# Kernel tuning notes

Measured on AMD Instinct MI355X. Metric: run time of the kernel, lower is better.

The kernel has to match this reference:

```python
import jax, jax.numpy as jnp
import numpy as np

B, D_IN, H, D_OUT = 1024, 64, 128, 16


def setup_inputs() -> dict:
    key = jax.random.key(0)
    k0, k1, k2 = jax.random.split(key, 3)
    x = jax.random.normal(k0, (B, D_IN), dtype=jnp.float32)
    W1 = jax.random.normal(k1, (D_IN, H), dtype=jnp.float32) / np.sqrt(D_IN).astype(np.float32)
    b1 = jnp.zeros((H,), dtype=jnp.float32)
    W2 = jax.random.normal(k2, (H, D_OUT), dtype=jnp.float32) / np.sqrt(H).astype(np.float32)
    b2 = jnp.zeros((D_OUT,), dtype=jnp.float32)
    return {"x": x, "W1": W1, "b1": b1, "W2": W2, "b2": b2}


def reference(x, W1, b1, W2, b2):
    # Wrapped net: 2-layer tanh MLP (hessQuik NN equivalent).
    def f_single(xi):  # xi: [D_IN] -> [D_OUT]
        return jnp.tanh(xi @ W1 + b1) @ W2 + b2

    # f: [B, D_OUT]  (torch: f.view(B, -1))
    f = jax.vmap(f_single)(x)

    # Torch builds df[b, i, j] = d f_j / d x_i via one grad per output column;
    # one reverse sweep per output == jacrev, vmapped over batch.
    J = jax.vmap(jax.jacrev(f_single))(x)            # [B, D_OUT, D_IN]
    df = jnp.transpose(J, (0, 2, 1))                 # [B, D_IN, D_OUT]

    # Torch builds d2f[b, k, i, j] = d^2 f_j / (d x_k d x_i); symmetric in (k, i).
    Hs = jax.vmap(jax.hessian(f_single))(x)          # [B, D_OUT, D_IN, D_IN]
    d2f = jnp.transpose(Hs, (0, 2, 3, 1))            # [B, D_IN, D_IN, D_OUT]

    return f, df, d2f
```

## Files before the change

kernel.cpp:

```cpp
#include <hip/hip_runtime.h>
#include <hip/hip_bf16.h>


typedef unsigned short u16;
typedef short s8v __attribute__((ext_vector_type(8)));
typedef float f4v __attribute__((ext_vector_type(4)));

__device__ __forceinline__ u16 f2bf(float f){
  __hip_bfloat16 h = __float2bfloat16(f);
  return __builtin_bit_cast(u16, h);
}

#define W1S 132

__global__ __launch_bounds__(256) void k_all(
    const float* __restrict__ x, const float* __restrict__ W1, const float* __restrict__ b1,
    const float* __restrict__ W2, const float* __restrict__ b2,
    float* __restrict__ f_out, float* __restrict__ df_out, float* __restrict__ d2f)
{
  const int tid  = threadIdx.x;
  const int lane = tid & 63;
  const int wave = tid >> 6;
  const int n = lane & 15;
  const int q = lane >> 4;
  const int b0 = blockIdx.x * 4;
  const int mb = blockIdx.y;

  __shared__ float sW1[64 * W1S];
  __shared__ __align__(16) float sGF[4096];
  __shared__ float sx[256];
  u16* sG = (u16*)sGF;

#pragma unroll
  for (int v = 0; v < 8; ++v){
    int idx = v*256 + tid;
    int r = idx >> 5;
    int c = (idx & 31) << 2;
    *(f4v*)&sW1[r*W1S + c] = *(const f4v*)&W1[r*128 + c];
  }
  sx[tid] = x[b0*64 + tid];
  __syncthreads();

  float a_keep = 0.f, s_keep = 0.f;
#pragma unroll
  for (int it = 0; it < 2; ++it){
    int idx = it*256 + tid;
    int s = idx >> 7;
    int h = idx & 127;
    float z = b1[h];
#pragma unroll 8
    for (int i = 0; i < 64; ++i) z += sx[s*64 + i] * sW1[i*W1S + h];
    float a = tanhf(z);
    float sd = 1.0f - a*a;
    float t = -2.0f * a * sd;
    if (it == mb){ a_keep = a; s_keep = sd; }
    f4v w2r[4];
#pragma unroll
    for (int v2 = 0; v2 < 4; ++v2) w2r[v2] = *(const f4v*)&W2[h*16 + v2*4];
#pragma unroll
    for (int j = 0; j < 16; ++j){
      int byte = (j*256 + h*2) ^ ((j & 7) << 4);
      sG[s*2048 + (byte >> 1)] = f2bf(t * w2r[j >> 2][j & 3]);
    }
  }
  __syncthreads();

  s8v bfrag[4][4];
#pragma unroll
  for (int s = 0; s < 4; ++s){
#pragma unroll
    for (int ks = 0; ks < 4; ++ks){
      int byte = (n*256 + q*16 + ks*64) ^ ((n & 7) << 4);
      bfrag[s][ks] = *(const s8v*)&sG[s*2048 + (byte >> 1)];
    }
  }
  __syncthreads();

  {
    const int ls = tid >> 7;
    const int h  = tid & 127;
    float* sF = sGF;
    sx[tid] = a_keep;
    f4v w2r[4];
#pragma unroll
    for (int v2 = 0; v2 < 4; ++v2) w2r[v2] = *(const f4v*)&W2[h*16 + v2*4];
#pragma unroll
    for (int v2 = 0; v2 < 4; ++v2){
      f4v sv;
#pragma unroll
      for (int e = 0; e < 4; ++e) sv[e] = s_keep * w2r[v2][e];
      *(f4v*)&sF[ls*2048 + h*16 + v2*4] = sv;
    }
    __syncthreads();

    const int sub = tid & 127;
    const int i   = sub >> 1;
    const int j0  = (sub & 1) * 8;
    const int bS  = b0 + 2*mb + ls;
    float acc[8] = {0,0,0,0,0,0,0,0};
    for (int h0 = 0; h0 < 128; h0 += 8){
      const float4* wp = (const float4*)&W1[i*128 + h0];
      float4 wa = wp[0], wb = wp[1];
      float wf[8] = {wa.x, wa.y, wa.z, wa.w, wb.x, wb.y, wb.z, wb.w};
#pragma unroll
      for (int hh = 0; hh < 8; ++hh){
        const f4v* sp = (const f4v*)&sF[ls*2048 + (h0 + hh)*16 + j0];
        f4v A = sp[0], Bv = sp[1];
        float w1 = wf[hh];
        acc[0] += w1*A[0];  acc[1] += w1*A[1];  acc[2] += w1*A[2];  acc[3] += w1*A[3];
        acc[4] += w1*Bv[0]; acc[5] += w1*Bv[1]; acc[6] += w1*Bv[2]; acc[7] += w1*Bv[3];
      }
    }
    f4v v0 = {acc[0], acc[1], acc[2], acc[3]};
    f4v v1 = {acc[4], acc[5], acc[6], acc[7]};
    float* dp = &df_out[bS*1024 + i*16 + j0];
    __builtin_nontemporal_store(v0, (f4v*)dp);
    __builtin_nontemporal_store(v1, (f4v*)(dp + 4));

    if (sub < 16){
      float accf = b2[sub];
      for (int h2 = 0; h2 < 128; ++h2) accf += sx[ls*128 + h2] * W2[h2*16 + sub];
      __builtin_nontemporal_store(accf, &f_out[bS*16 + sub]);
    }
  }

  const int R0 = mb*2048 + wave*512;
#pragma unroll 2
  for (int mt = 0; mt < 32; ++mt){
    const int rowbase = R0 + mt*16;
    const int r = rowbase + n;
    const int i = r & 63;
    const int k = r >> 6;
    const float* wi = &sW1[i*W1S];
    const float* wk = &sW1[k*W1S];
    s8v afrag[4];
#pragma unroll
    for (int ks = 0; ks < 4; ++ks){
      int c = q*8 + ks*32;
      f4v ia = *(const f4v*)&wi[c];
      f4v ib = *(const f4v*)&wi[c+4];
      f4v ka = *(const f4v*)&wk[c];
      f4v kb = *(const f4v*)&wk[c+4];
      s8v av;
#pragma unroll
      for (int e = 0; e < 4; ++e) av[e]   = (short)f2bf(ia[e]*ka[e]);
#pragma unroll
      for (int e = 0; e < 4; ++e) av[4+e] = (short)f2bf(ib[e]*kb[e]);
      afrag[ks] = av;
    }
#pragma unroll
    for (int s = 0; s < 4; ++s){
      f4v acc = {0.f, 0.f, 0.f, 0.f};
#pragma unroll
      for (int ks = 0; ks < 4; ++ks)
        acc = __builtin_amdgcn_mfma_f32_16x16x32_bf16(bfrag[s][ks], afrag[ks], acc, 0, 0, 0);
      float* op = d2f + (size_t)(b0 + s)*65536 + (size_t)(rowbase + n)*16 + q*4;
      *(f4v*)op = acc;
    }
  }
}

extern "C" void kernel_launch(void* const* d_in, const int* in_sizes, int n_in,
                              void* d_out, int out_size, void* d_ws, size_t ws_size,
                              hipStream_t stream)
{
  (void)in_sizes; (void)n_in; (void)out_size; (void)d_ws; (void)ws_size;
  const float* x  = (const float*)d_in[0];
  const float* W1 = (const float*)d_in[1];
  const float* b1 = (const float*)d_in[2];
  const float* W2 = (const float*)d_in[3];
  const float* b2 = (const float*)d_in[4];

  float* out     = (float*)d_out;
  float* f_out   = out;
  float* df_out  = out + 16384;
  float* d2f_out = out + 1064960;

  k_all<<<dim3(256, 2), 256, 0, stream>>>(x, W1, b1, W2, b2, f_out, df_out, d2f_out);
}
```

Baseline: 276.3 us.

## Exploit Hessian symmetry to compute only lower-triangular blocks and mirror stores

The d2f loop now computes only the diagonal and lower-triangular 16x16 (k,i) blocks, chosen from packed block tables. Off-diagonal results are written to both (k,i) and (i,k), which cuts MFMA and A-fragment work nearly in half. Each iteration also handles two adjacent k rows, sharing the i-row loads, and launch bounds now request two blocks per CU. The kernel appears bound by stores of the large d2f output, and the store volume is unchanged, so the compute savings may matter little. The mirrored stores are also less coalesced.

```diff
diff --git a/kernel.cpp b/kernel.cpp
--- a/kernel.cpp
+++ b/kernel.cpp
@@ -13,7 +13,7 @@
 
 #define W1S 132
 
-__global__ __launch_bounds__(256) void k_all(
+__global__ __launch_bounds__(256, 2) void k_all(
     const float* __restrict__ x, const float* __restrict__ W1, const float* __restrict__ b1,
     const float* __restrict__ W2, const float* __restrict__ b2,
     float* __restrict__ f_out, float* __restrict__ df_out, float* __restrict__ d2f)
@@ -124,38 +124,59 @@
     }
   }
 
-  const int R0 = mb*2048 + wave*512;
+  const int w8 = mb*4 + wave;
+  const size_t sB0 = (size_t)b0 * 65536;
 #pragma unroll 2
-  for (int mt = 0; mt < 32; ++mt){
-    const int rowbase = R0 + mt*16;
-    const int r = rowbase + n;
-    const int i = r & 63;
-    const int k = r >> 6;
-    const float* wi = &sW1[i*W1S];
-    const float* wk = &sW1[k*W1S];
-    s8v afrag[4];
+  for (int pp = 0; pp < 10; ++pp){
+    const int p   = w8*10 + pp;
+    const int blk = p >> 3;
+    const int kk2 = (p & 7) * 2;
+    const int KB  = (int)((0x2110003210ULL >> (4*blk)) & 15);
+    const int IB  = (int)((0x3323213210ULL >> (4*blk)) & 15);
+    const int k   = KB*16 + kk2;
+    const int I0  = IB*16;
+    const bool diag = (blk < 4);
+
+    const int i = I0 + n;
+    const float* wi  = &sW1[i*W1S];
+    const float* wkA = &sW1[k*W1S];
+    const float* wkB = &sW1[(k+1)*W1S];
+    s8v afK[4], afK1[4];
 #pragma unroll
     for (int ks = 0; ks < 4; ++ks){
       int c = q*8 + ks*32;
       f4v ia = *(const f4v*)&wi[c];
       f4v ib = *(const f4v*)&wi[c+4];
-      f4v ka = *(const f4v*)&wk[c];
-      f4v kb = *(const f4v*)&wk[c+4];
-      s8v av;
-#pragma unroll
-      for (int e = 0; e < 4; ++e) av[e]   = (short)f2bf(ia[e]*ka[e]);
-#pragma unroll
-      for (int e = 0; e < 4; ++e) av[4+e] = (short)f2bf(ib[e]*kb[e]);
-      afrag[ks] = av;
+      f4v ka = *(const f4v*)&wkA[c];
+      f4v kb = *(const f4v*)&wkA[c+4];
+      f4v kc = *(const f4v*)&wkB[c];
+      f4v kd = *(const f4v*)&wkB[c+4];
+      s8v a0, a1;
+#pragma unroll
+      for (int e = 0; e < 4; ++e){
+        a0[e]   = (short)f2bf(ia[e]*ka[e]);
+        a0[4+e] = (short)f2bf(ib[e]*kb[e]);
+        a1[e]   = (short)f2bf(ia[e]*kc[e]);
+        a1[4+e] = (short)f2bf(ib[e]*kd[e]);
+      }
+      afK[ks] = a0; afK1[ks] = a1;
     }
 #pragma unroll
     for (int s = 0; s < 4; ++s){
-      f4v acc = {0.f, 0.f, 0.f, 0.f};
-#pragma unroll
-      for (int ks = 0; ks < 4; ++ks)
-        acc = __builtin_amdgcn_mfma_f32_16x16x32_bf16(bfrag[s][ks], afrag[ks], acc, 0, 0, 0);
-      float* op = d2f + (size_t)(b0 + s)*65536 + (size_t)(rowbase + n)*16 + q*4;
-      *(f4v*)op = acc;
+      f4v accK = {0.f,0.f,0.f,0.f}, accK1 = {0.f,0.f,0.f,0.f};
+#pragma unroll
+      for (int ks = 0; ks < 4; ++ks){
+        accK  = __builtin_amdgcn_mfma_f32_16x16x32_bf16(bfrag[s][ks], afK[ks],  accK,  0, 0, 0);
+        accK1 = __builtin_amdgcn_mfma_f32_16x16x32_bf16(bfrag[s][ks], afK1[ks], accK1, 0, 0, 0);
+      }
+      float* baseS = d2f + sB0 + (size_t)s*65536;
+      *(f4v*)(baseS + (size_t)(k*64 + i)*16 + q*4)       = accK;
+      *(f4v*)(baseS + (size_t)((k+1)*64 + i)*16 + q*4)   = accK1;
+      if (!diag){
+        float* mp = baseS + (size_t)(i*64 + k)*16 + q*4;
+        *(f4v*)mp        = accK;
+        *(f4v*)(mp + 16) = accK1;
+      }
     }
   }
 }
```

Result: no change. 277.5 us (+0.4%).
